# Kernel tuning notes

Hardware: AMD Instinct MI355X
Metric: run time of the kernel (lower is better)

Reference implementation:

```python
import jax, jax.numpy as jnp
import numpy as np

N = 50000      # nodes
E = 800000     # edges (avg degree 16)
G = 256        # graphs in batch
IN = 128       # in_channels
H = 256        # hidden_channels
L = 4          # num_layers


def setup_inputs() -> dict:
    key = jax.random.key(0)
    ks = jax.random.split(key, 16)
    x = jax.random.normal(ks[0], (N, IN), dtype=jnp.float32)
    edge_index = jax.random.randint(ks[1], (2, E), 0, N, dtype=jnp.int64)
    batch = jnp.sort(jax.random.randint(ks[2], (N,), 0, G, dtype=jnp.int64))
    s_in = 1.0 / np.sqrt(IN)
    s_h = 1.0 / np.sqrt(H)
    return {
        "x": x,
        "edge_index": edge_index,
        "batch": batch,
        "w1_0": jax.random.normal(ks[3], (IN, H), jnp.float32) * s_in,
        "b1_0": jnp.zeros((H,), jnp.float32),
        "w2_0": jax.random.normal(ks[4], (H, H), jnp.float32) * s_h,
        "b2_0": jnp.zeros((H,), jnp.float32),
        "w1s": jax.random.normal(ks[5], (L - 1, H, H), jnp.float32) * s_h,
        "b1s": jnp.zeros((L - 1, H), jnp.float32),
        "w2s": jax.random.normal(ks[6], (L - 1, H, H), jnp.float32) * s_h,
        "b2s": jnp.zeros((L - 1, H), jnp.float32),
    }


def reference(x, edge_index, batch, w1_0, b1_0, w2_0, b2_0, w1s, b1s, w2s, b2s):
    n_nodes = x.shape[0]
    src, dst = edge_index[0], edge_index[1]

    def gin_layer(h, w1, b1, w2, b2):
        # scatter-add neighbor aggregation: out[i] = sum_{(j->i)} h[j]
        agg = jax.ops.segment_sum(h[src], dst, num_segments=n_nodes)
        z = h + agg  # GIN with eps = 0: (1+eps)*x + aggr
        z = jax.nn.relu(z @ w1 + b1) @ w2 + b2  # MLP: Linear-ReLU-Linear
        return jax.nn.relu(z)  # outer F.relu in forward

    h = gin_layer(x, w1_0, b1_0, w2_0, b2_0)
    for i in range(L - 1):  # small fixed layer loop
        h = gin_layer(h, w1s[i], b1s[i], w2s[i], b2s[i])

    # global_add_pool: per-graph segment sum -> [G, H]
    return jax.ops.segment_sum(h, batch, num_segments=G)
```

## Files before the change

kernel.cpp:

```cpp
#include <hip/hip_runtime.h>
#include <hip/hip_bf16.h>

#define NN 50000
#define NE 800000
#define NG 256
#define CIN 128
#define CH 256
#define CAP 64

typedef unsigned short u16;
typedef unsigned int u32;
typedef unsigned char u8;
typedef __attribute__((ext_vector_type(8))) short short8;
typedef __attribute__((ext_vector_type(8))) unsigned short ushort8;
typedef __attribute__((ext_vector_type(4))) float f32x4;

__device__ __forceinline__ float bf2f(u16 u) { return __uint_as_float(((u32)u) << 16); }
__device__ __forceinline__ u16 f2bf(float f) {
    u32 u = __float_as_uint(f);
    return (u16)((u + 0x7fffu + ((u >> 16) & 1u)) >> 16);
}

__global__ void k_prep(const float* __restrict__ x, u16* __restrict__ xb,
                       const float* __restrict__ w1_0, const float* __restrict__ w2_0,
                       const float* __restrict__ w1s, const float* __restrict__ w2s,
                       u16* __restrict__ Wp, int* __restrict__ deg,
                       float* __restrict__ outf, float* __restrict__ S) {
    int t = blockIdx.x * 256 + threadIdx.x;
    if (t < NN) deg[t] = 0;
    if (t < NG * CH) outf[t] = 0.f;
    if (t < CIN) xb[(size_t)NN * CIN + t] = 0;
    if (t == 0) S[NN] = 0.f;
    if (t < NN * CIN / 4) {
        float4 v = ((const float4*)x)[t];
        ushort4 o; o.x = f2bf(v.x); o.y = f2bf(v.y); o.z = f2bf(v.z); o.w = f2bf(v.w);
        ((ushort4*)xb)[t] = o;
    }
    if (t < CIN * CH + 7 * CH * CH) {
        const float* Wsrc; int rem;
        if (t < CIN * CH) { Wsrc = w1_0; rem = t; }
        else {
            int o = t - CIN * CH;
            int m = o >> 16; rem = o & 65535;
            Wsrc = (m == 0) ? w2_0
                 : (m <= 3) ? w1s + (size_t)(m - 1) * 65536
                            : w2s + (size_t)(m - 4) * 65536;
        }
        int j = rem & 7, lane = (rem >> 3) & 63, nt = (rem >> 9) & 15, kb = rem >> 13;
        int k = kb * 32 + ((lane >> 4) << 3) + j;
        int nc = nt * 16 + (lane & 15);
        Wp[t] = f2bf(Wsrc[k * CH + nc]);
    }
}

__global__ void k_build(const int* __restrict__ dst, const int* __restrict__ src,
                        int* __restrict__ deg, u16* __restrict__ colu) {
    int t = blockIdx.x * 256 + threadIdx.x;
    if (t < NE / 4) {
        int4 d4 = ((const int4*)dst)[t];
        int4 s4 = ((const int4*)src)[t];
        int dd[4] = {d4.x, d4.y, d4.z, d4.w};
        int ss[4] = {s4.x, s4.y, s4.z, s4.w};
#pragma unroll
        for (int u = 0; u < 4; u++) {
            int pos = atomicAdd(&deg[dd[u]], 1);
            colu[dd[u] * CAP + pos] = (u16)ss[u];
        }
    }
}

__global__ __launch_bounds__(256, 8) void k_gather_x(const u16* __restrict__ xb,
                                                     const int* __restrict__ deg,
                                                     const u16* __restrict__ colu,
                                                     u16* __restrict__ Z) {
    const int lane = threadIdx.x & 63;
    const int r = __builtin_amdgcn_readfirstlane(blockIdx.x * 4 + (threadIdx.x >> 6));
    const int co = lane * 2;
    u32 sv = *(const u32*)(xb + (size_t)r * CIN + co);
    float a0 = __uint_as_float(sv << 16);
    float a1 = __uint_as_float(sv & 0xffff0000u);
    const int dg = deg[r];
    const u16* cb = colu + r * CAP;
    for (int e = 0; e < dg; e += 8) {
        ushort8 cv = *(const ushort8*)(cb + e);
        int idx[8];
#pragma unroll
        for (int u = 0; u < 8; u++) {
            int id = (e + u < dg) ? (int)cv[u] : NN;
            idx[u] = __builtin_amdgcn_readfirstlane(id);
        }
        u32 qw[8];
#pragma unroll
        for (int u = 0; u < 8; u++)
            qw[u] = *(const u32*)(xb + (size_t)idx[u] * CIN + co);
#pragma unroll
        for (int u = 0; u < 8; u++) {
            a0 += __uint_as_float(qw[u] << 16);
            a1 += __uint_as_float(qw[u] & 0xffff0000u);
        }
    }
    u32 o = (u32)f2bf(a0) | ((u32)f2bf(a1) << 16);
    *(u32*)(Z + (size_t)r * CIN + co) = o;
}

__global__ __launch_bounds__(256, 8) void k_gather_q(const u16* __restrict__ G,
                                                     const u8* __restrict__ Qin,
                                                     const float* __restrict__ Sin,
                                                     const int* __restrict__ deg,
                                                     const u16* __restrict__ colu,
                                                     u16* __restrict__ Z) {
    const int lane = threadIdx.x & 63;
    const int r = __builtin_amdgcn_readfirstlane(blockIdx.x * 4 + (threadIdx.x >> 6));
    const int co = lane * 4;
    ushort4 sv = *(const ushort4*)(G + (size_t)r * CH + co);
    float a0 = bf2f(sv.x), a1 = bf2f(sv.y), a2 = bf2f(sv.z), a3 = bf2f(sv.w);
    const int dg = deg[r];
    const u16* cb = colu + r * CAP;
    for (int e = 0; e < dg; e += 8) {
        ushort8 cv = *(const ushort8*)(cb + e);
        int idx[8]; float sc[8];
#pragma unroll
        for (int u = 0; u < 8; u++) {
            int id = (e + u < dg) ? (int)cv[u] : NN;
            idx[u] = __builtin_amdgcn_readfirstlane(id);
            sc[u] = Sin[idx[u]];
        }
        u32 qw[8];
#pragma unroll
        for (int u = 0; u < 8; u++)
            qw[u] = *(const u32*)(Qin + (size_t)idx[u] * CH + co);
#pragma unroll
        for (int u = 0; u < 8; u++) {
            a0 += sc[u] * (float)(qw[u] & 0xffu);
            a1 += sc[u] * (float)((qw[u] >> 8) & 0xffu);
            a2 += sc[u] * (float)((qw[u] >> 16) & 0xffu);
            a3 += sc[u] * (float)(qw[u] >> 24);
        }
    }
    ushort4 o; o.x = f2bf(a0); o.y = f2bf(a1); o.z = f2bf(a2); o.w = f2bf(a3);
    *(ushort4*)(Z + (size_t)r * CH + co) = o;
}

#define ZS 264
template <int K1, bool QOUT, bool POOL>
__global__ __launch_bounds__(256, 6) void k_layer(const u16* __restrict__ Z,
                                                  const u16* __restrict__ Wp1,
                                                  const float* __restrict__ b1,
                                                  const u16* __restrict__ Wp2,
                                                  const float* __restrict__ b2,
                                                  u16* __restrict__ out,
                                                  u8* __restrict__ Qout,
                                                  float* __restrict__ Sout,
                                                  const int* __restrict__ batchp,
                                                  float* __restrict__ outf) {
    __shared__ __align__(16) u16 zs[32 * ZS];
    const int tid = threadIdx.x;
    const int wave = tid >> 6, lane = tid & 63;
    const int quad = lane >> 4, l16 = lane & 15;
    const int m0 = blockIdx.x * 32;

    {
        int row = tid >> 3, ccb = (tid & 7) * (K1 / 8);
        int r = m0 + row; if (r >= NN) r = NN - 1;
        const u16* zp = Z + (size_t)r * K1 + ccb;
        u16* zd = zs + row * ZS + ccb;
#pragma unroll
        for (int c = 0; c < K1 / 64; c++)
            *(ushort8*)(zd + c * 8) = *(const ushort8*)(zp + c * 8);
    }
    __syncthreads();

    f32x4 acc[2][4];
#pragma unroll
    for (int ri = 0; ri < 2; ri++)
#pragma unroll
        for (int nj = 0; nj < 4; nj++) acc[ri][nj] = (f32x4){0.f, 0.f, 0.f, 0.f};

    const u16* w1b = Wp1 + (wave * 4) * 512 + lane * 8;
    const u16* w2b = Wp2 + (wave * 4) * 512 + lane * 8;
    constexpr int KB1 = K1 / 32;
    short8 b_cur[4], b_nxt[4];
#pragma unroll
    for (int nj = 0; nj < 4; nj++) b_cur[nj] = *(const short8*)(w1b + nj * 512);

#pragma unroll
    for (int kb = 0; kb < KB1; kb++) {
        int kn = (kb + 1 < KB1) ? (kb + 1) : kb;
#pragma unroll
        for (int nj = 0; nj < 4; nj++)
            b_nxt[nj] = *(const short8*)(w1b + kn * 8192 + nj * 512);
        short8 a[2];
#pragma unroll
        for (int ri = 0; ri < 2; ri++)
            a[ri] = *(const short8*)(zs + (ri * 16 + l16) * ZS + kb * 32 + quad * 8);
#pragma unroll
        for (int nj = 0; nj < 4; nj++)
#pragma unroll
            for (int ri = 0; ri < 2; ri++)
                acc[ri][nj] = __builtin_amdgcn_mfma_f32_16x16x32_bf16(a[ri], b_cur[nj], acc[ri][nj], 0, 0, 0);
#pragma unroll
        for (int nj = 0; nj < 4; nj++) b_cur[nj] = b_nxt[nj];
    }

    short8 b2_cur[4];
#pragma unroll
    for (int nj = 0; nj < 4; nj++) b2_cur[nj] = *(const short8*)(w2b + nj * 512);

    __syncthreads();

#pragma unroll
    for (int nj = 0; nj < 4; nj++) {
        int cc = wave * 64 + nj * 16 + l16;
        float bv = b1[cc];
#pragma unroll
        for (int ri = 0; ri < 2; ri++) {
            f32x4 v = acc[ri][nj];
#pragma unroll
            for (int j = 0; j < 4; j++)
                zs[(ri * 16 + quad * 4 + j) * ZS + cc] = f2bf(fmaxf(v[j] + bv, 0.f));
        }
    }
    __syncthreads();

#pragma unroll
    for (int ri = 0; ri < 2; ri++)
#pragma unroll
        for (int nj = 0; nj < 4; nj++) acc[ri][nj] = (f32x4){0.f, 0.f, 0.f, 0.f};

#pragma unroll
    for (int kb = 0; kb < 8; kb++) {
        int kn = (kb + 1 < 8) ? (kb + 1) : kb;
#pragma unroll
        for (int nj = 0; nj < 4; nj++)
            b_nxt[nj] = *(const short8*)(w2b + kn * 8192 + nj * 512);
        short8 a[2];
#pragma unroll
        for (int ri = 0; ri < 2; ri++)
            a[ri] = *(const short8*)(zs + (ri * 16 + l16) * ZS + kb * 32 + quad * 8);
#pragma unroll
        for (int nj = 0; nj < 4; nj++)
#pragma unroll
            for (int ri = 0; ri < 2; ri++)
                acc[ri][nj] = __builtin_amdgcn_mfma_f32_16x16x32_bf16(a[ri], b2_cur[nj], acc[ri][nj], 0, 0, 0);
#pragma unroll
        for (int nj = 0; nj < 4; nj++) b2_cur[nj] = b_nxt[nj];
    }
    __syncthreads();

#pragma unroll
    for (int nj = 0; nj < 4; nj++) {
        int cc = wave * 64 + nj * 16 + l16;
        float bv = b2[cc];
#pragma unroll
        for (int ri = 0; ri < 2; ri++) {
            f32x4 v = acc[ri][nj];
#pragma unroll
            for (int j = 0; j < 4; j++)
                zs[(ri * 16 + quad * 4 + j) * ZS + cc] = f2bf(fmaxf(v[j] + bv, 0.f));
        }
    }
    __syncthreads();

    if (!POOL) {
        int row = tid >> 3, cb = (tid & 7) * 32;
        int r = m0 + row;
        if (r < NN) {
            uint4* dst = (uint4*)(out + (size_t)r * CH + cb);
            const u16* srcp = zs + row * ZS + cb;
#pragma unroll
            for (int c = 0; c < 4; c++) dst[c] = *(const uint4*)(srcp + c * 8);
            if (QOUT) {
                float vloc[32]; float mx = 0.f;
#pragma unroll
                for (int c = 0; c < 32; c++) { vloc[c] = bf2f(srcp[c]); mx = fmaxf(mx, vloc[c]); }
                mx = fmaxf(mx, __shfl_xor(mx, 1));
                mx = fmaxf(mx, __shfl_xor(mx, 2));
                mx = fmaxf(mx, __shfl_xor(mx, 4));
                float inv = mx > 0.f ? 255.f / mx : 0.f;
                u32 qw[8];
#pragma unroll
                for (int d = 0; d < 8; d++) {
                    u32 q0 = (u32)(vloc[d * 4 + 0] * inv + 0.5f);
                    u32 q1 = (u32)(vloc[d * 4 + 1] * inv + 0.5f);
                    u32 q2 = (u32)(vloc[d * 4 + 2] * inv + 0.5f);
                    u32 q3 = (u32)(vloc[d * 4 + 3] * inv + 0.5f);
                    qw[d] = q0 | (q1 << 8) | (q2 << 16) | (q3 << 24);
                }
                uint4* qdst = (uint4*)(Qout + (size_t)r * CH + cb);
                qdst[0] = *(const uint4*)&qw[0];
                qdst[1] = *(const uint4*)&qw[4];
                if ((tid & 7) == 0) Sout[r] = mx * (1.f / 255.f);
            }
        }
    } else {
        int c = tid;
        float acc2 = 0.f;
        int cur_g = batchp[m0];
        for (int row = 0; row < 32; row++) {
            int r = m0 + row;
            if (r >= NN) break;
            int g = batchp[r];
            if (g != cur_g) {
                atomicAdd(&outf[cur_g * CH + c], acc2);
                acc2 = 0.f; cur_g = g;
            }
            acc2 += bf2f(zs[row * ZS + c]);
        }
        atomicAdd(&outf[cur_g * CH + c], acc2);
    }
}

extern "C" void kernel_launch(void* const* d_in, const int* in_sizes, int n_in,
                              void* d_out, int out_size, void* d_ws, size_t ws_size,
                              hipStream_t stream) {
    const float* x     = (const float*)d_in[0];
    const int*   ei    = (const int*)d_in[1];
    const int*   batch = (const int*)d_in[2];
    const float* w1_0  = (const float*)d_in[3];
    const float* b1_0  = (const float*)d_in[4];
    const float* w2_0  = (const float*)d_in[5];
    const float* b2_0  = (const float*)d_in[6];
    const float* w1s   = (const float*)d_in[7];
    const float* b1s   = (const float*)d_in[8];
    const float* w2s   = (const float*)d_in[9];
    const float* b2s   = (const float*)d_in[10];
    float* out = (float*)d_out;

    char* p = (char*)d_ws;
    u16* Hb  = (u16*)p; p += (size_t)NN * CH * 2;
    u16* Zb  = (u16*)p; p += (size_t)NN * CH * 2;
    u16* xb  = (u16*)p; p += (size_t)(NN + 1) * CIN * 2;
    u16* WpA = (u16*)p; p += (size_t)(CIN * CH + 7 * CH * CH) * 2;
    int* deg = (int*)p; p += (size_t)NN * 4;
    u16* colu= (u16*)p; p += (size_t)NN * CAP * 2;
    u8*  Qb  = (u8*)p;  p += (size_t)(NN + 1) * CH;
    float* Sb= (float*)p; p += (size_t)(NN + 1) * 4;

    u16* Wp1_0 = WpA;
    u16* Wp2_0 = Wp1_0 + CIN * CH;
    u16* Wp1sA = Wp2_0 + CH * CH;
    u16* Wp2sA = Wp1sA + 3 * CH * CH;

    const int* srcv = ei;
    const int* dstv = ei + NE;

    int gatherBlocks = NN / 4;
    int layerBlocks  = (NN + 31) / 32;

    hipLaunchKernelGGL(k_prep, dim3((NN * CIN / 4 + 255) / 256), dim3(256), 0, stream,
                       x, xb, w1_0, w2_0, w1s, w2s, WpA, deg, out, Sb);

    hipLaunchKernelGGL(k_build, dim3((NE / 4 + 255) / 256), dim3(256), 0, stream,
                       dstv, srcv, deg, colu);

    hipLaunchKernelGGL(k_gather_x, dim3(gatherBlocks), dim3(256), 0, stream,
                       xb, deg, colu, Zb);
    hipLaunchKernelGGL((k_layer<128, true, false>), dim3(layerBlocks), dim3(256), 0, stream,
                       Zb, Wp1_0, b1_0, Wp2_0, b2_0, Hb, Qb, Sb, batch, out);

    hipLaunchKernelGGL(k_gather_q, dim3(gatherBlocks), dim3(256), 0, stream,
                       Hb, Qb, Sb, deg, colu, Zb);
    hipLaunchKernelGGL((k_layer<256, true, false>), dim3(layerBlocks), dim3(256), 0, stream,
                       Zb, Wp1sA, b1s, Wp2sA, b2s, Hb, Qb, Sb, batch, out);

    hipLaunchKernelGGL(k_gather_q, dim3(gatherBlocks), dim3(256), 0, stream,
                       Hb, Qb, Sb, deg, colu, Zb);
    hipLaunchKernelGGL((k_layer<256, true, false>), dim3(layerBlocks), dim3(256), 0, stream,
                       Zb, Wp1sA + (size_t)CH * CH, b1s + CH,
                       Wp2sA + (size_t)CH * CH, b2s + CH, Hb, Qb, Sb, batch, out);

    hipLaunchKernelGGL(k_gather_q, dim3(gatherBlocks), dim3(256), 0, stream,
                       Hb, Qb, Sb, deg, colu, Zb);
    hipLaunchKernelGGL((k_layer<256, false, true>), dim3(layerBlocks), dim3(256), 0, stream,
                       Zb, Wp1sA + (size_t)2 * CH * CH, b1s + 2 * CH,
                       Wp2sA + (size_t)2 * CH * CH, b2s + 2 * CH,
                       (u16*)nullptr, (u8*)nullptr, (float*)nullptr, batch, out);
}
```

Baseline: 422.9 us.

## Split neighbor gathers into two column-half passes and use nontemporal streaming

Each gather kernel now runs twice, each pass covering half of the feature columns, so the randomly accessed source table per pass is half as wide and more of it can stay in cache. Outputs and layer-kernel Z loads/stores use nontemporal hints so streaming data does not evict the gathered tables. The edge-list build reverts to one edge per thread. The cost is reading the CSR index lists and degrees twice, issuing narrower per-lane loads, and launching more kernels.

After: 503.8 us. 19.1% more time.

```diff
diff --git a/kernel.cpp b/kernel.cpp
--- a/kernel.cpp
+++ b/kernel.cpp
@@ -14,6 +14,7 @@
 typedef __attribute__((ext_vector_type(8))) short short8;
 typedef __attribute__((ext_vector_type(8))) unsigned short ushort8;
 typedef __attribute__((ext_vector_type(4))) float f32x4;
+typedef __attribute__((ext_vector_type(4))) unsigned int u32x4;
 
 __device__ __forceinline__ float bf2f(u16 u) { return __uint_as_float(((u32)u) << 16); }
 __device__ __forceinline__ u16 f2bf(float f) {
@@ -55,69 +56,58 @@
 
 __global__ void k_build(const int* __restrict__ dst, const int* __restrict__ src,
                         int* __restrict__ deg, u16* __restrict__ colu) {
-    int t = blockIdx.x * 256 + threadIdx.x;
-    if (t < NE / 4) {
-        int4 d4 = ((const int4*)dst)[t];
-        int4 s4 = ((const int4*)src)[t];
-        int dd[4] = {d4.x, d4.y, d4.z, d4.w};
-        int ss[4] = {s4.x, s4.y, s4.z, s4.w};
-#pragma unroll
-        for (int u = 0; u < 4; u++) {
-            int pos = atomicAdd(&deg[dd[u]], 1);
-            colu[dd[u] * CAP + pos] = (u16)ss[u];
-        }
+    int e = blockIdx.x * 256 + threadIdx.x;
+    if (e < NE) {
+        int d = dst[e];
+        int pos = atomicAdd(&deg[d], 1);
+        colu[d * CAP + pos] = (u16)src[e];
     }
 }
 
 __global__ __launch_bounds__(256, 8) void k_gather_x(const u16* __restrict__ xb,
                                                      const int* __restrict__ deg,
                                                      const u16* __restrict__ colu,
-                                                     u16* __restrict__ Z) {
+                                                     u16* __restrict__ Z, int coBase) {
     const int lane = threadIdx.x & 63;
     const int r = __builtin_amdgcn_readfirstlane(blockIdx.x * 4 + (threadIdx.x >> 6));
-    const int co = lane * 2;
-    u32 sv = *(const u32*)(xb + (size_t)r * CIN + co);
+    const int co = coBase + lane;
+    float a = bf2f(xb[(size_t)r * CIN + co]);
+    const int dg = deg[r];
+    const u16* cb = colu + r * CAP;
+    for (int e = 0; e < dg; e += 8) {
+        ushort8 cv = *(const ushort8*)(cb + e);
+        int idx[8];
+#pragma unroll
+        for (int u = 0; u < 8; u++) {
+            int id = (e + u < dg) ? (int)cv[u] : NN;
+            idx[u] = __builtin_amdgcn_readfirstlane(id);
+        }
+        u16 qw[8];
+#pragma unroll
+        for (int u = 0; u < 8; u++)
+            qw[u] = xb[(size_t)idx[u] * CIN + co];
+#pragma unroll
+        for (int u = 0; u < 8; u++) a += bf2f(qw[u]);
+    }
+    __builtin_nontemporal_store(f2bf(a), Z + (size_t)r * CIN + co);
+}
+
+__global__ __launch_bounds__(256, 8) void k_gather_q(const u16* __restrict__ G,
+                                                     const u8* __restrict__ Qin,
+                                                     const float* __restrict__ Sin,
+                                                     const int* __restrict__ deg,
+                                                     const u16* __restrict__ colu,
+                                                     u16* __restrict__ Z, int coBase) {
+    const int lane = threadIdx.x & 63;
+    const int r = __builtin_amdgcn_readfirstlane(blockIdx.x * 4 + (threadIdx.x >> 6));
+    const int co = coBase + lane * 2;
+    u32 sv = *(const u32*)(G + (size_t)r * CH + co);
     float a0 = __uint_as_float(sv << 16);
     float a1 = __uint_as_float(sv & 0xffff0000u);
     const int dg = deg[r];
     const u16* cb = colu + r * CAP;
     for (int e = 0; e < dg; e += 8) {
         ushort8 cv = *(const ushort8*)(cb + e);
-        int idx[8];
-#pragma unroll
-        for (int u = 0; u < 8; u++) {
-            int id = (e + u < dg) ? (int)cv[u] : NN;
-            idx[u] = __builtin_amdgcn_readfirstlane(id);
-        }
-        u32 qw[8];
-#pragma unroll
-        for (int u = 0; u < 8; u++)
-            qw[u] = *(const u32*)(xb + (size_t)idx[u] * CIN + co);
-#pragma unroll
-        for (int u = 0; u < 8; u++) {
-            a0 += __uint_as_float(qw[u] << 16);
-            a1 += __uint_as_float(qw[u] & 0xffff0000u);
-        }
-    }
-    u32 o = (u32)f2bf(a0) | ((u32)f2bf(a1) << 16);
-    *(u32*)(Z + (size_t)r * CIN + co) = o;
-}
-
-__global__ __launch_bounds__(256, 8) void k_gather_q(const u16* __restrict__ G,
-                                                     const u8* __restrict__ Qin,
-                                                     const float* __restrict__ Sin,
-                                                     const int* __restrict__ deg,
-                                                     const u16* __restrict__ colu,
-                                                     u16* __restrict__ Z) {
-    const int lane = threadIdx.x & 63;
-    const int r = __builtin_amdgcn_readfirstlane(blockIdx.x * 4 + (threadIdx.x >> 6));
-    const int co = lane * 4;
-    ushort4 sv = *(const ushort4*)(G + (size_t)r * CH + co);
-    float a0 = bf2f(sv.x), a1 = bf2f(sv.y), a2 = bf2f(sv.z), a3 = bf2f(sv.w);
-    const int dg = deg[r];
-    const u16* cb = colu + r * CAP;
-    for (int e = 0; e < dg; e += 8) {
-        ushort8 cv = *(const ushort8*)(cb + e);
         int idx[8]; float sc[8];
 #pragma unroll
         for (int u = 0; u < 8; u++) {
@@ -125,20 +115,18 @@
             idx[u] = __builtin_amdgcn_readfirstlane(id);
             sc[u] = Sin[idx[u]];
         }
-        u32 qw[8];
+        u16 qw[8];
 #pragma unroll
         for (int u = 0; u < 8; u++)
-            qw[u] = *(const u32*)(Qin + (size_t)idx[u] * CH + co);
+            qw[u] = *(const u16*)(Qin + (size_t)idx[u] * CH + co);
 #pragma unroll
         for (int u = 0; u < 8; u++) {
             a0 += sc[u] * (float)(qw[u] & 0xffu);
-            a1 += sc[u] * (float)((qw[u] >> 8) & 0xffu);
-            a2 += sc[u] * (float)((qw[u] >> 16) & 0xffu);
-            a3 += sc[u] * (float)(qw[u] >> 24);
-        }
-    }
-    ushort4 o; o.x = f2bf(a0); o.y = f2bf(a1); o.z = f2bf(a2); o.w = f2bf(a3);
-    *(ushort4*)(Z + (size_t)r * CH + co) = o;
+            a1 += sc[u] * (float)(qw[u] >> 8);
+        }
+    }
+    u32 o = (u32)f2bf(a0) | ((u32)f2bf(a1) << 16);
+    __builtin_nontemporal_store(o, (u32*)(Z + (size_t)r * CH + co));
 }
 
 #define ZS 264
@@ -162,11 +150,11 @@
     {
         int row = tid >> 3, ccb = (tid & 7) * (K1 / 8);
         int r = m0 + row; if (r >= NN) r = NN - 1;
-        const u16* zp = Z + (size_t)r * K1 + ccb;
+        const u32x4* zp = (const u32x4*)(Z + (size_t)r * K1 + ccb);
         u16* zd = zs + row * ZS + ccb;
 #pragma unroll
         for (int c = 0; c < K1 / 64; c++)
-            *(ushort8*)(zd + c * 8) = *(const ushort8*)(zp + c * 8);
+            *(u32x4*)(zd + c * 8) = __builtin_nontemporal_load(zp + c);
     }
     __syncthreads();
 
@@ -265,10 +253,11 @@
         int row = tid >> 3, cb = (tid & 7) * 32;
         int r = m0 + row;
         if (r < NN) {
-            uint4* dst = (uint4*)(out + (size_t)r * CH + cb);
+            u32x4* dst = (u32x4*)(out + (size_t)r * CH + cb);
             const u16* srcp = zs + row * ZS + cb;
 #pragma unroll
-            for (int c = 0; c < 4; c++) dst[c] = *(const uint4*)(srcp + c * 8);
+            for (int c = 0; c < 4; c++)
+                __builtin_nontemporal_store(*(const u32x4*)(srcp + c * 8), dst + c);
             if (QOUT) {
                 float vloc[32]; float mx = 0.f;
 #pragma unroll
@@ -277,18 +266,19 @@
                 mx = fmaxf(mx, __shfl_xor(mx, 2));
                 mx = fmaxf(mx, __shfl_xor(mx, 4));
                 float inv = mx > 0.f ? 255.f / mx : 0.f;
-                u32 qw[8];
+                u32x4 qa, qb;
 #pragma unroll
                 for (int d = 0; d < 8; d++) {
                     u32 q0 = (u32)(vloc[d * 4 + 0] * inv + 0.5f);
                     u32 q1 = (u32)(vloc[d * 4 + 1] * inv + 0.5f);
                     u32 q2 = (u32)(vloc[d * 4 + 2] * inv + 0.5f);
                     u32 q3 = (u32)(vloc[d * 4 + 3] * inv + 0.5f);
-                    qw[d] = q0 | (q1 << 8) | (q2 << 16) | (q3 << 24);
+                    u32 qw = q0 | (q1 << 8) | (q2 << 16) | (q3 << 24);
+                    if (d < 4) qa[d] = qw; else qb[d - 4] = qw;
                 }
-                uint4* qdst = (uint4*)(Qout + (size_t)r * CH + cb);
-                qdst[0] = *(const uint4*)&qw[0];
-                qdst[1] = *(const uint4*)&qw[4];
+                u32x4* qdst = (u32x4*)(Qout + (size_t)r * CH + cb);
+                __builtin_nontemporal_store(qa, qdst);
+                __builtin_nontemporal_store(qb, qdst + 1);
                 if ((tid & 7) == 0) Sout[r] = mx * (1.f / 255.f);
             }
         }
@@ -350,27 +340,35 @@
     hipLaunchKernelGGL(k_prep, dim3((NN * CIN / 4 + 255) / 256), dim3(256), 0, stream,
                        x, xb, w1_0, w2_0, w1s, w2s, WpA, deg, out, Sb);
 
-    hipLaunchKernelGGL(k_build, dim3((NE / 4 + 255) / 256), dim3(256), 0, stream,
+    hipLaunchKernelGGL(k_build, dim3((NE + 255) / 256), dim3(256), 0, stream,
                        dstv, srcv, deg, colu);
 
     hipLaunchKernelGGL(k_gather_x, dim3(gatherBlocks), dim3(256), 0, stream,
-                       xb, deg, colu, Zb);
+                       xb, deg, colu, Zb, 0);
+    hipLaunchKernelGGL(k_gather_x, dim3(gatherBlocks), dim3(256), 0, stream,
+                       xb, deg, colu, Zb, 64);
     hipLaunchKernelGGL((k_layer<128, true, false>), dim3(layerBlocks), dim3(256), 0, stream,
                        Zb, Wp1_0, b1_0, Wp2_0, b2_0, Hb, Qb, Sb, batch, out);
 
     hipLaunchKernelGGL(k_gather_q, dim3(gatherBlocks), dim3(256), 0, stream,
-                       Hb, Qb, Sb, deg, colu, Zb);
+                       Hb, Qb, Sb, deg, colu, Zb, 0);
+    hipLaunchKernelGGL(k_gather_q, dim3(gatherBlocks), dim3(256), 0, stream,
+                       Hb, Qb, Sb, deg, colu, Zb, 128);
     hipLaunchKernelGGL((k_layer<256, true, false>), dim3(layerBlocks), dim3(256), 0, stream,
                        Zb, Wp1sA, b1s, Wp2sA, b2s, Hb, Qb, Sb, batch, out);
 
     hipLaunchKernelGGL(k_gather_q, dim3(gatherBlocks), dim3(256), 0, stream,
-                       Hb, Qb, Sb, deg, colu, Zb);
+                       Hb, Qb, Sb, deg, colu, Zb, 0);
+    hipLaunchKernelGGL(k_gather_q, dim3(gatherBlocks), dim3(256), 0, stream,
+                       Hb, Qb, Sb, deg, colu, Zb, 128);
     hipLaunchKernelGGL((k_layer<256, true, false>), dim3(layerBlocks), dim3(256), 0, stream,
                        Zb, Wp1sA + (size_t)CH * CH, b1s + CH,
                        Wp2sA + (size_t)CH * CH, b2s + CH, Hb, Qb, Sb, batch, out);
 
     hipLaunchKernelGGL(k_gather_q, dim3(gatherBlocks), dim3(256), 0, stream,
-                       Hb, Qb, Sb, deg, colu, Zb);
+                       Hb, Qb, Sb, deg, colu, Zb, 0);
+    hipLaunchKernelGGL(k_gather_q, dim3(gatherBlocks), dim3(256), 0, stream,
+                       Hb, Qb, Sb, deg, colu, Zb, 128);
     hipLaunchKernelGGL((k_layer<256, false, true>), dim3(layerBlocks), dim3(256), 0, stream,
                        Zb, Wp1sA + (size_t)2 * CH * CH, b1s + 2 * CH,
                        Wp2sA + (size_t)2 * CH * CH, b2s + 2 * CH,
```
